# Performance work log

Measured on AMD Instinct MI355X. Metric: run time of the kernel, lower is better.

## Reference

```python
import jax, jax.numpy as jnp
import numpy as np

V = 8000; TZ = 128; TU = 256; B = 64; H = 1024; E = 512; DG = 64
GI = E + 2 * H + DG  # GRU input size = embed + z_ctx + u_ctx + degree


def _build_sparse_z(rng):
    # faithful vectorized version of get_sparse_selective_input (minus vocab SLOT branch)
    z_np = rng.integers(0, V + 10, size=(TZ, B))  # some ids >= V -> OOV copy path
    res = np.full((TZ, B, V + TZ), 1e-10, np.float32)
    w = z_np[:-1]                                   # [TZ-1, B]
    cond = (w == 2) | (w >= V)
    ti, bi = np.meshgrid(np.arange(TZ - 1), np.arange(B), indexing='ij')
    col = np.where(cond, V + ti, w)
    val = np.where(cond, np.float32(5.0), np.float32(1.0))
    res[ti + 1, bi, col] = val
    return jnp.asarray(res.transpose(1, 0, 2))      # [B, TZ, V+TZ]


def setup_inputs():
    key = jax.random.key(0)
    ks = jax.random.split(key, 16)
    s = 0.02
    iv = 1.0 / np.sqrt(H)
    return dict(
        z_enc_out=jax.random.normal(ks[0], (TZ, B, H), jnp.float32),
        u_enc_out=jax.random.normal(ks[1], (TU, B, H), jnp.float32),
        m_t_input=jax.random.randint(ks[2], (1, B), 0, V),
        degree_input=jax.random.normal(ks[3], (B, DG), jnp.float32),
        last_hidden=jax.random.normal(ks[4], (1, B, H), jnp.float32),
        sparse_z_input=_build_sparse_z(np.random.default_rng(0)),
        emb_W=jax.random.normal(ks[5], (V, E), jnp.float32) * s,
        attn_z_W=jax.random.normal(ks[6], (H, 2 * H), jnp.float32) * s,
        attn_z_b=jnp.zeros((H,), jnp.float32),
        attn_z_v=jax.random.normal(ks[7], (H,), jnp.float32) * iv,
        attn_u_W=jax.random.normal(ks[8], (H, 2 * H), jnp.float32) * s,
        attn_u_b=jnp.zeros((H,), jnp.float32),
        attn_u_v=jax.random.normal(ks[9], (H,), jnp.float32) * iv,
        gru_Wih=jax.random.normal(ks[10], (3 * H, GI), jnp.float32) * s,
        gru_Whh=jax.random.normal(ks[11], (3 * H, H), jnp.float32) * s,
        gru_bih=jnp.zeros((3 * H,), jnp.float32),
        gru_bhh=jnp.zeros((3 * H,), jnp.float32),
        proj_W=jax.random.normal(ks[12], (V, 3 * H), jnp.float32) * s,
        proj_b=jnp.zeros((V,), jnp.float32),
        copy2_W=jax.random.normal(ks[13], (H, H), jnp.float32) * s,
        copy2_b=jnp.zeros((H,), jnp.float32),
    )


def _attn(hidden, enc, W, b, v):
    # hidden [1,B,H], enc [T,B,H] -> context [1,B,H] (Bahdanau additive attention)
    enc_b = jnp.transpose(enc, (1, 0, 2))                       # [B,T,H]
    Hrep = jnp.broadcast_to(jnp.transpose(hidden, (1, 0, 2)), enc_b.shape)
    energy = jnp.tanh(jnp.concatenate([Hrep, enc_b], -1) @ W.T + b)  # [B,T,H]
    scores = jnp.einsum('bth,h->bt', energy, v)[:, None, :]    # [B,1,T]
    alpha = jax.nn.softmax(scores, axis=2)
    ctx = jnp.einsum('bit,bth->bih', alpha, enc_b)              # [B,1,H]
    return jnp.transpose(ctx, (1, 0, 2))                        # [1,B,H]


def _gru_step(x, h, Wih, Whh, bih, bhh):
    # single step, torch gate order (r, z, n)
    gi = x @ Wih.T + bih
    gh = h @ Whh.T + bhh
    ir, iz, inn = jnp.split(gi, 3, -1)
    hr, hz, hn = jnp.split(gh, 3, -1)
    r = jax.nn.sigmoid(ir + hr)
    z = jax.nn.sigmoid(iz + hz)
    n = jnp.tanh(inn + r * hn)
    return (1.0 - z) * n + z * h


def reference(z_enc_out, u_enc_out, m_t_input, degree_input, last_hidden,
              sparse_z_input, emb_W, attn_z_W, attn_z_b, attn_z_v,
              attn_u_W, attn_u_b, attn_u_v, gru_Wih, gru_Whh, gru_bih, gru_bhh,
              proj_W, proj_b, copy2_W, copy2_b):
    m_embed = emb_W[m_t_input]                                  # [1,B,E]
    z_ctx = _attn(last_hidden, z_enc_out, attn_z_W, attn_z_b, attn_z_v)  # [1,B,H]
    u_ctx = _attn(last_hidden, u_enc_out, attn_u_W, attn_u_b, attn_u_v)  # [1,B,H]
    gru_in = jnp.concatenate([m_embed, u_ctx, z_ctx, degree_input[None]], axis=2)
    gru_out = _gru_step(gru_in, last_hidden, gru_Wih, gru_Whh, gru_bih, gru_bhh)
    new_hidden = gru_out                                        # single-layer GRU, 1 step
    gen_score = (jnp.concatenate([z_ctx, u_ctx, gru_out], 2) @ proj_W.T + proj_b)[0]  # [B,V]
    # pointer copy scores over z encoder states
    z_cs = jnp.tanh(jnp.transpose(z_enc_out, (1, 0, 2)) @ copy2_W.T + copy2_b)  # [B,TZ,H]
    z_cs = jnp.einsum('bth,bh->bt', z_cs, gru_out[0])           # [B,TZ]
    m = jnp.max(z_cs, axis=1, keepdims=True)
    e = jnp.exp(z_cs - m)
    z_copy = jnp.log(jnp.einsum('bt,btv->bv', e, sparse_z_input)) + m  # [B,V+TZ]
    scores = jax.nn.softmax(jnp.concatenate([gen_score, z_copy], axis=1), axis=1)
    gen_s, zc = scores[:, :V], scores[:, V:]
    proba = jnp.concatenate([gen_s + zc[:, :V], zc[:, V:]], axis=1)  # [B, V+TZ]
    return (proba, new_hidden, gru_out)
```

## Files before the change

### kernel.cpp

```cpp
#include <hip/hip_runtime.h>
#include <cmath>

#define B64 64
#define H 1024
#define E 512
#define DG 64
#define GIN 2624
#define TZ 128
#define TU 256
#define V 8000
#define VT 8128
#define NC 16128

using bf16x8 = __attribute__((ext_vector_type(8))) short;
using f32x4  = __attribute__((ext_vector_type(4))) float;

__device__ inline unsigned pack2(float a, float b) {
    unsigned ua = __float_as_uint(a) + 0x8000u;
    unsigned ub = __float_as_uint(b) + 0x8000u;
    return __builtin_amdgcn_perm(ub, ua, 0x07060302u);
}
__device__ inline uint2 pack4(float4 v) {
    return make_uint2(pack2(v.x, v.y), pack2(v.z, v.w));
}

__device__ inline void gl_lds16(const void* gptr, void* lptr) {
    __builtin_amdgcn_global_load_lds(
        (const __attribute__((address_space(1))) void*)gptr,
        (__attribute__((address_space(3))) void*)lptr, 16, 0, 0);
}

__global__ void k_cvt(const float* __restrict__ src, int ld, int koff,
                      unsigned short* __restrict__ dst)
{
    int n = blockIdx.x, k4 = threadIdx.x * 4;
    float4 v = *(const float4*)(src + (size_t)n * ld + koff + k4);
    *(uint2*)(dst + (size_t)n * 1024 + k4) = pack4(v);
}

__global__ __launch_bounds__(256) void fused_tanh_dot_bf(
    const unsigned short* __restrict__ A,
    const unsigned short* __restrict__ W,
    const float* __restrict__ addv, int add_stride,
    const float* __restrict__ multv, int mult_stride,
    float* __restrict__ outs)
{
    __shared__ unsigned short As[128 * 32];
    __shared__ unsigned short Bs[128 * 32];
    const int tid  = threadIdx.x;
    const int wave = tid >> 6, lane = tid & 63;
    const int wm = wave >> 1, wn = wave & 1;
    const int q = lane >> 4, l16 = lane & 15;
    const int m0 = blockIdx.x * 128;
    const int n0 = blockIdx.y * 128;
    const int lrow = lane >> 2;
    const int lk   = (lane & 3) * 8;

    f32x4 acc[4][4];
#pragma unroll
    for (int i = 0; i < 4; ++i)
#pragma unroll
        for (int j = 0; j < 4; ++j) acc[i][j] = f32x4{0.f, 0.f, 0.f, 0.f};

    for (int kt = 0; kt < 32; ++kt) {
        const int k0 = kt * 32;
        __syncthreads();
#pragma unroll
        for (int j = 0; j < 2; ++j) {
            int r0 = (wave * 2 + j) * 16;
            gl_lds16(A + (size_t)(m0 + r0 + lrow) * 1024 + k0 + lk, &As[r0 * 32]);
            gl_lds16(W + (size_t)(n0 + r0 + lrow) * 1024 + k0 + lk, &Bs[r0 * 32]);
        }
        __syncthreads();
        bf16x8 af[4], bfr[4];
#pragma unroll
        for (int t = 0; t < 4; ++t) af[t]  = *(bf16x8*)&As[(wm * 64 + t * 16 + l16) * 32 + q * 8];
#pragma unroll
        for (int t = 0; t < 4; ++t) bfr[t] = *(bf16x8*)&Bs[(wn * 64 + t * 16 + l16) * 32 + q * 8];
#pragma unroll
        for (int tm = 0; tm < 4; ++tm)
#pragma unroll
            for (int tn = 0; tn < 4; ++tn)
                acc[tm][tn] = __builtin_amdgcn_mfma_f32_16x16x32_bf16(
                    af[tm], bfr[tn], acc[tm][tn], 0, 0, 0);
    }

#pragma unroll
    for (int tm = 0; tm < 4; ++tm) {
#pragma unroll
        for (int r = 0; r < 4; ++r) {
            int R = m0 + wm * 64 + tm * 16 + q * 4 + r;
            int b = R & 63;
            float s = 0.f;
#pragma unroll
            for (int tn = 0; tn < 4; ++tn) {
                int col = n0 + wn * 64 + tn * 16 + l16;
                float e = acc[tm][tn][r] + addv[(size_t)b * add_stride + col];
                s += tanhf(e) * multv[(size_t)b * mult_stride + col];
            }
            s += __shfl_xor(s, 1);
            s += __shfl_xor(s, 2);
            s += __shfl_xor(s, 4);
            s += __shfl_xor(s, 8);
            if (l16 == 0) atomicAdd(&outs[R], s);
        }
    }
}

__global__ __launch_bounds__(256) void gemm_bt_mfma(
    const float* __restrict__ A, int lda,
    const float* __restrict__ W, int ldw, int koff,
    const float* __restrict__ bias,
    float* __restrict__ C, int N,
    int ks_total, int ks_chunk)
{
    __shared__ short As[64][40];
    __shared__ short Bs[64][40];
    const int tid  = threadIdx.x;
    const int wave = tid >> 6, lane = tid & 63;
    const int wm = wave >> 1, wn = wave & 1;
    const int q = lane >> 4, l16 = lane & 15;
    const int n0 = blockIdx.x * 64;
    const int kb = blockIdx.y * ks_chunk;
    const int ke = min(kb + ks_chunk, ks_total);

    f32x4 acc[2][2];
#pragma unroll
    for (int i = 0; i < 2; ++i)
#pragma unroll
        for (int j = 0; j < 2; ++j) acc[i][j] = f32x4{0.f, 0.f, 0.f, 0.f};

    for (int ks = kb; ks < ke; ++ks) {
        const int k0 = ks * 32;
        __syncthreads();
#pragma unroll
        for (int i = 0; i < 2; ++i) {
            int slot = i * 256 + tid;
            int row  = slot >> 3;
            int kq   = (slot & 7) << 2;
            float4 a = *(const float4*)(A + (size_t)row * lda + k0 + kq);
            *(uint2*)&As[row][kq] = pack4(a);
            float4 w = *(const float4*)(W + (size_t)(n0 + row) * ldw + koff + k0 + kq);
            *(uint2*)&Bs[row][kq] = pack4(w);
        }
        __syncthreads();
        bf16x8 af[2], bfr[2];
#pragma unroll
        for (int t = 0; t < 2; ++t) af[t]  = *(bf16x8*)&As[wm * 32 + t * 16 + l16][q * 8];
#pragma unroll
        for (int t = 0; t < 2; ++t) bfr[t] = *(bf16x8*)&Bs[wn * 32 + t * 16 + l16][q * 8];
#pragma unroll
        for (int tm = 0; tm < 2; ++tm)
#pragma unroll
            for (int tn = 0; tn < 2; ++tn)
                acc[tm][tn] = __builtin_amdgcn_mfma_f32_16x16x32_bf16(
                    af[tm], bfr[tn], acc[tm][tn], 0, 0, 0);
    }

#pragma unroll
    for (int tm = 0; tm < 2; ++tm) {
#pragma unroll
        for (int r = 0; r < 4; ++r) {
            int b = wm * 32 + tm * 16 + q * 4 + r;
#pragma unroll
            for (int tn = 0; tn < 2; ++tn) {
                int n = n0 + wn * 32 + tn * 16 + l16;
                float v = acc[tm][tn][r];
                if (blockIdx.y == 0) v += bias[n];
                atomicAdd(&C[(size_t)b * N + n], v);
            }
        }
    }
}

__global__ void k_gather(const int* __restrict__ mt, const float* __restrict__ embW,
                         const float* __restrict__ degree, float* __restrict__ x)
{
    int b = blockIdx.x, tid = threadIdx.x;
    int m = mt[b];
    for (int k = tid; k < E; k += 128) x[(size_t)b * GIN + k] = embW[(size_t)m * E + k];
    if (tid < DG) x[(size_t)b * GIN + E + 2 * H + tid] = degree[b * DG + tid];
}

__global__ __launch_bounds__(256) void k_softmax_ctx(
    const float* __restrict__ scores, const float* __restrict__ enc, int T,
    float* __restrict__ x, int xoff, float* __restrict__ y, int yoff)
{
    __shared__ float red[256];
    __shared__ float al[256];
    int b = blockIdx.x, hc = blockIdx.y, tid = threadIdx.x;
    float s = (tid < T) ? scores[tid * B64 + b] : -1e30f;
    red[tid] = s; __syncthreads();
    for (int off = 128; off > 0; off >>= 1) {
        if (tid < off) red[tid] = fmaxf(red[tid], red[tid + off]);
        __syncthreads();
    }
    float mx = red[0]; __syncthreads();
    float e = (tid < T) ? expf(s - mx) : 0.f;
    red[tid] = e; __syncthreads();
    for (int off = 128; off > 0; off >>= 1) {
        if (tid < off) red[tid] += red[tid + off];
        __syncthreads();
    }
    float inv = 1.f / red[0];
    al[tid] = e * inv;
    __syncthreads();
    int h = hc * 256 + tid;
    float acc = 0.f;
    for (int t = 0; t < T; ++t) acc += al[t] * enc[((size_t)t * B64 + b) * H + h];
    x[(size_t)b * GIN + xoff + h] = acc;
    y[(size_t)b * 3072 + yoff + h] = acc;
}

__global__ void k_gate(const float* __restrict__ gi, const float* __restrict__ gh,
                       const float* __restrict__ h0, float* __restrict__ gru,
                       float* __restrict__ y, float* __restrict__ out_hid,
                       float* __restrict__ out_gru)
{
    int b = blockIdx.x, tid = threadIdx.x;
    for (int j = tid; j < H; j += 256) {
        float ir = gi[(size_t)b * 3072 + j];
        float iz = gi[(size_t)b * 3072 + H + j];
        float in_ = gi[(size_t)b * 3072 + 2 * H + j];
        float hr = gh[(size_t)b * 3072 + j];
        float hz = gh[(size_t)b * 3072 + H + j];
        float hn = gh[(size_t)b * 3072 + 2 * H + j];
        float r = 1.f / (1.f + expf(-(ir + hr)));
        float z = 1.f / (1.f + expf(-(iz + hz)));
        float n = tanhf(in_ + r * hn);
        float h = h0[(size_t)b * H + j];
        float o = (1.f - z) * n + z * h;
        gru[(size_t)b * H + j] = o;
        y[(size_t)b * 3072 + 2 * H + j] = o;
        out_hid[(size_t)b * H + j] = o;
        out_gru[(size_t)b * H + j] = o;
    }
}

__global__ void k_expw(const float* __restrict__ z_cs, float* __restrict__ ew,
                       float* __restrict__ mb)
{
    __shared__ float red[128];
    int b = blockIdx.x, t = threadIdx.x;
    float s = z_cs[t * B64 + b];
    red[t] = s; __syncthreads();
    for (int off = 64; off > 0; off >>= 1) {
        if (t < off) red[t] = fmaxf(red[t], red[t + off]);
        __syncthreads();
    }
    float m = red[0];
    ew[b * TZ + t] = expf(s - m);
    if (t == 0) mb[b] = m;
}

__global__ __launch_bounds__(256) void k_sparse(
    const float* __restrict__ sz, const float* __restrict__ ew,
    const float* __restrict__ mb, float* __restrict__ zcopy)
{
    __shared__ float es[TZ];
    int c = blockIdx.x, b = blockIdx.y, tid = threadIdx.x;
    if (tid < TZ) es[tid] = ew[b * TZ + tid];
    __syncthreads();
    if (tid >= 254) return;
    int v4 = c * 254 + tid;
    const float4* base = (const float4*)(sz + (size_t)b * TZ * VT);
    float4 acc = make_float4(0.f, 0.f, 0.f, 0.f);
    for (int t = 0; t < TZ; ++t) {
        float4 xv = base[(size_t)t * (VT / 4) + v4];
        float e = es[t];
        acc.x += e * xv.x; acc.y += e * xv.y; acc.z += e * xv.z; acc.w += e * xv.w;
    }
    float m = mb[b];
    int v = v4 * 4;
    zcopy[(size_t)b * VT + v + 0] = logf(acc.x) + m;
    zcopy[(size_t)b * VT + v + 1] = logf(acc.y) + m;
    zcopy[(size_t)b * VT + v + 2] = logf(acc.z) + m;
    zcopy[(size_t)b * VT + v + 3] = logf(acc.w) + m;
}

__global__ __launch_bounds__(1024) void k_final(
    const float* __restrict__ gen, const float* __restrict__ zcopy,
    float* __restrict__ proba)
{
    __shared__ float lg[NC];
    __shared__ float wred[16];
    int b = blockIdx.x, tid = threadIdx.x;
    int lane = tid & 63, wave = tid >> 6;
    for (int i = tid; i < V; i += 1024) lg[i] = gen[(size_t)b * V + i];
    for (int i = tid; i < VT; i += 1024) lg[V + i] = zcopy[(size_t)b * VT + i];
    __syncthreads();
    float mx = -1e30f;
    for (int i = tid; i < NC; i += 1024) mx = fmaxf(mx, lg[i]);
#pragma unroll
    for (int off = 32; off > 0; off >>= 1) mx = fmaxf(mx, __shfl_xor(mx, off));
    if (lane == 0) wred[wave] = mx;
    __syncthreads();
    mx = wred[0];
#pragma unroll
    for (int w = 1; w < 16; ++w) mx = fmaxf(mx, wred[w]);
    __syncthreads();
    float sm = 0.f;
    for (int i = tid; i < NC; i += 1024) sm += expf(lg[i] - mx);
#pragma unroll
    for (int off = 32; off > 0; off >>= 1) sm += __shfl_xor(sm, off);
    if (lane == 0) wred[wave] = sm;
    __syncthreads();
    float Z = 0.f;
#pragma unroll
    for (int w = 0; w < 16; ++w) Z += wred[w];
    float invZ = 1.f / Z;
    for (int v = tid; v < VT; v += 1024) {
        float p = expf(lg[V + v] - mx) * invZ;
        if (v < V) p += expf(lg[v] - mx) * invZ;
        proba[(size_t)b * VT + v] = p;
    }
}

extern "C" void kernel_launch(void* const* d_in, const int* in_sizes, int n_in,
                              void* d_out, int out_size, void* d_ws, size_t ws_size,
                              hipStream_t stream)
{
    const float* z_enc  = (const float*)d_in[0];
    const float* u_enc  = (const float*)d_in[1];
    const int*   mt     = (const int*)d_in[2];
    const float* degree = (const float*)d_in[3];
    const float* h0     = (const float*)d_in[4];
    const float* sz     = (const float*)d_in[5];
    const float* embW   = (const float*)d_in[6];
    const float* azW    = (const float*)d_in[7];
    const float* azb    = (const float*)d_in[8];
    const float* azv    = (const float*)d_in[9];
    const float* auW    = (const float*)d_in[10];
    const float* aub    = (const float*)d_in[11];
    const float* auv    = (const float*)d_in[12];
    const float* Wih    = (const float*)d_in[13];
    const float* Whh    = (const float*)d_in[14];
    const float* bih    = (const float*)d_in[15];
    const float* bhh    = (const float*)d_in[16];
    const float* pW     = (const float*)d_in[17];
    const float* pb     = (const float*)d_in[18];
    const float* c2W    = (const float*)d_in[19];
    const float* c2b    = (const float*)d_in[20];

    float* ws       = (float*)d_ws;
    float* scores_z = ws;
    float* scores_u = ws + 8192;
    float* z_cs     = ws + 24576;
    float* hbz      = ws + 32768;
    float* hbu      = ws + 98304;
    float* gi       = ws + 163840;
    float* gh       = ws + 360448;
    float* gen      = ws + 557056;
    float* x        = ws + 1069056;
    float* y        = ws + 1236992;
    float* gru      = ws + 1433600;
    float* ew       = ws + 1499136;
    float* mb       = ws + 1507328;
    float* zcopy    = ws + 1507392;
    unsigned short* ubf   = (unsigned short*)(ws + 2027584);
    unsigned short* zbf   = ubf + (size_t)16384 * 1024;
    unsigned short* azWbf = zbf + (size_t)8192 * 1024;
    unsigned short* auWbf = azWbf + (size_t)1024 * 1024;
    unsigned short* c2Wbf = auWbf + (size_t)1024 * 1024;

    float* out_proba = (float*)d_out;
    float* out_hid   = out_proba + (size_t)B64 * VT;
    float* out_gru   = out_hid + (size_t)B64 * H;

    hipMemsetAsync(ws, 0, 1069056 * sizeof(float), stream);

    k_cvt<<<16384, 256, 0, stream>>>(u_enc, 1024, 0, ubf);
    k_cvt<<<8192, 256, 0, stream>>>(z_enc, 1024, 0, zbf);
    k_cvt<<<1024, 256, 0, stream>>>(azW, 2048, 1024, azWbf);
    k_cvt<<<1024, 256, 0, stream>>>(auW, 2048, 1024, auWbf);
    k_cvt<<<1024, 256, 0, stream>>>(c2W, 1024, 0, c2Wbf);

    gemm_bt_mfma<<<dim3(16, 4), 256, 0, stream>>>(h0, 1024, azW, 2048, 0, azb, hbz, 1024, 32, 8);
    gemm_bt_mfma<<<dim3(16, 4), 256, 0, stream>>>(h0, 1024, auW, 2048, 0, aub, hbu, 1024, 32, 8);
    k_gather<<<64, 128, 0, stream>>>(mt, embW, degree, x);
    gemm_bt_mfma<<<dim3(48, 4), 256, 0, stream>>>(h0, 1024, Whh, 1024, 0, bhh, gh, 3072, 32, 8);

    fused_tanh_dot_bf<<<dim3(64, 8), 256, 0, stream>>>(zbf, azWbf, hbz, 1024, azv, 0, scores_z);
    fused_tanh_dot_bf<<<dim3(128, 8), 256, 0, stream>>>(ubf, auWbf, hbu, 1024, auv, 0, scores_u);

    k_softmax_ctx<<<dim3(64, 4), 256, 0, stream>>>(scores_z, z_enc, TZ, x, 1536, y, 0);
    k_softmax_ctx<<<dim3(64, 4), 256, 0, stream>>>(scores_u, u_enc, TU, x, 512, y, 1024);

    gemm_bt_mfma<<<dim3(48, 4), 256, 0, stream>>>(x, GIN, Wih, GIN, 0, bih, gi, 3072, 82, 21);
    k_gate<<<64, 256, 0, stream>>>(gi, gh, h0, gru, y, out_hid, out_gru);

    fused_tanh_dot_bf<<<dim3(64, 8), 256, 0, stream>>>(zbf, c2Wbf, c2b, 0, gru, 1024, z_cs);

    gemm_bt_mfma<<<dim3(125, 3), 256, 0, stream>>>(y, 3072, pW, 3072, 0, pb, gen, 8000, 96, 32);

    k_expw<<<64, 128, 0, stream>>>(z_cs, ew, mb);
    k_sparse<<<dim3(8, 64), 256, 0, stream>>>(sz, ew, mb, zcopy);

    k_final<<<64, 1024, 0, stream>>>(gen, zcopy, out_proba);
}
```

Baseline: 864.4 us.

## Merge conversions, fuse z-attention with copy GEMM, read bf16 encoders, use fast math

```diff
diff --git a/kernel.cpp b/kernel.cpp
--- a/kernel.cpp
+++ b/kernel.cpp
@@ -24,18 +24,36 @@
     return make_uint2(pack2(v.x, v.y), pack2(v.z, v.w));
 }
 
+__device__ inline float fast_tanh(float x) {
+    float e = __expf(2.f * x);
+    return 1.f - 2.f / (e + 1.f);
+}
+__device__ inline float fast_sig(float x) {
+    return 1.f / (1.f + __expf(-x));
+}
+
 __device__ inline void gl_lds16(const void* gptr, void* lptr) {
     __builtin_amdgcn_global_load_lds(
         (const __attribute__((address_space(1))) void*)gptr,
         (__attribute__((address_space(3))) void*)lptr, 16, 0, 0);
 }
 
-__global__ void k_cvt(const float* __restrict__ src, int ld, int koff,
-                      unsigned short* __restrict__ dst)
+__global__ void k_cvt_all(const float* __restrict__ u_enc, const float* __restrict__ z_enc,
+                          const float* __restrict__ azW, const float* __restrict__ auW,
+                          const float* __restrict__ c2W,
+                          unsigned short* __restrict__ ubf, unsigned short* __restrict__ zbf,
+                          unsigned short* __restrict__ azWbf, unsigned short* __restrict__ auWbf,
+                          unsigned short* __restrict__ c2Wbf)
 {
     int n = blockIdx.x, k4 = threadIdx.x * 4;
-    float4 v = *(const float4*)(src + (size_t)n * ld + koff + k4);
-    *(uint2*)(dst + (size_t)n * 1024 + k4) = pack4(v);
+    const float* src; unsigned short* dst; int ld, koff, r;
+    if (n < 16384)      { src = u_enc; dst = ubf;   ld = 1024; koff = 0;    r = n; }
+    else if (n < 24576) { src = z_enc; dst = zbf;   ld = 1024; koff = 0;    r = n - 16384; }
+    else if (n < 25600) { src = azW;   dst = azWbf; ld = 2048; koff = 1024; r = n - 24576; }
+    else if (n < 26624) { src = auW;   dst = auWbf; ld = 2048; koff = 1024; r = n - 25600; }
+    else                { src = c2W;   dst = c2Wbf; ld = 1024; koff = 0;    r = n - 26624; }
+    float4 v = *(const float4*)(src + (size_t)r * ld + koff + k4);
+    *(uint2*)(dst + (size_t)r * 1024 + k4) = pack4(v);
 }
 
 __global__ __launch_bounds__(256) void fused_tanh_dot_bf(
@@ -96,13 +114,101 @@
             for (int tn = 0; tn < 4; ++tn) {
                 int col = n0 + wn * 64 + tn * 16 + l16;
                 float e = acc[tm][tn][r] + addv[(size_t)b * add_stride + col];
-                s += tanhf(e) * multv[(size_t)b * mult_stride + col];
+                s += fast_tanh(e) * multv[(size_t)b * mult_stride + col];
             }
             s += __shfl_xor(s, 1);
             s += __shfl_xor(s, 2);
             s += __shfl_xor(s, 4);
             s += __shfl_xor(s, 8);
             if (l16 == 0) atomicAdd(&outs[R], s);
+        }
+    }
+}
+
+__global__ __launch_bounds__(256) void ftd_z_combo(
+    const unsigned short* __restrict__ A,
+    const unsigned short* __restrict__ Wz,
+    const float* __restrict__ hbz, const float* __restrict__ azv,
+    float* __restrict__ scores,
+    const unsigned short* __restrict__ Wc,
+    const float* __restrict__ c2b,
+    float* __restrict__ tz)
+{
+    __shared__ unsigned short As[128 * 32];
+    __shared__ unsigned short Bs[128 * 32];
+    const int tid  = threadIdx.x;
+    const int wave = tid >> 6, lane = tid & 63;
+    const int wm = wave >> 1, wn = wave & 1;
+    const int q = lane >> 4, l16 = lane & 15;
+    const int m0 = blockIdx.x * 128;
+    const bool isz = blockIdx.y < 8;
+    const int n0 = (isz ? blockIdx.y : blockIdx.y - 8) * 128;
+    const unsigned short* W = isz ? Wz : Wc;
+    const int lrow = lane >> 2;
+    const int lk   = (lane & 3) * 8;
+
+    f32x4 acc[4][4];
+#pragma unroll
+    for (int i = 0; i < 4; ++i)
+#pragma unroll
+        for (int j = 0; j < 4; ++j) acc[i][j] = f32x4{0.f, 0.f, 0.f, 0.f};
+
+    for (int kt = 0; kt < 32; ++kt) {
+        const int k0 = kt * 32;
+        __syncthreads();
+#pragma unroll
+        for (int j = 0; j < 2; ++j) {
+            int r0 = (wave * 2 + j) * 16;
+            gl_lds16(A + (size_t)(m0 + r0 + lrow) * 1024 + k0 + lk, &As[r0 * 32]);
+            gl_lds16(W + (size_t)(n0 + r0 + lrow) * 1024 + k0 + lk, &Bs[r0 * 32]);
+        }
+        __syncthreads();
+        bf16x8 af[4], bfr[4];
+#pragma unroll
+        for (int t = 0; t < 4; ++t) af[t]  = *(bf16x8*)&As[(wm * 64 + t * 16 + l16) * 32 + q * 8];
+#pragma unroll
+        for (int t = 0; t < 4; ++t) bfr[t] = *(bf16x8*)&Bs[(wn * 64 + t * 16 + l16) * 32 + q * 8];
+#pragma unroll
+        for (int tm = 0; tm < 4; ++tm)
+#pragma unroll
+            for (int tn = 0; tn < 4; ++tn)
+                acc[tm][tn] = __builtin_amdgcn_mfma_f32_16x16x32_bf16(
+                    af[tm], bfr[tn], acc[tm][tn], 0, 0, 0);
+    }
+
+    if (isz) {
+#pragma unroll
+        for (int tm = 0; tm < 4; ++tm) {
+#pragma unroll
+            for (int r = 0; r < 4; ++r) {
+                int R = m0 + wm * 64 + tm * 16 + q * 4 + r;
+                int b = R & 63;
+                float s = 0.f;
+#pragma unroll
+                for (int tn = 0; tn < 4; ++tn) {
+                    int col = n0 + wn * 64 + tn * 16 + l16;
+                    float e = acc[tm][tn][r] + hbz[(size_t)b * 1024 + col];
+                    s += fast_tanh(e) * azv[col];
+                }
+                s += __shfl_xor(s, 1);
+                s += __shfl_xor(s, 2);
+                s += __shfl_xor(s, 4);
+                s += __shfl_xor(s, 8);
+                if (l16 == 0) atomicAdd(&scores[R], s);
+            }
+        }
+    } else {
+#pragma unroll
+        for (int tm = 0; tm < 4; ++tm) {
+#pragma unroll
+            for (int r = 0; r < 4; ++r) {
+                int R = m0 + wm * 64 + tm * 16 + q * 4 + r;
+#pragma unroll
+                for (int tn = 0; tn < 4; ++tn) {
+                    int col = n0 + wn * 64 + tn * 16 + l16;
+                    tz[(size_t)R * 1024 + col] = fast_tanh(acc[tm][tn][r] + c2b[col]);
+                }
+            }
         }
     }
 }
@@ -182,8 +288,8 @@
     if (tid < DG) x[(size_t)b * GIN + E + 2 * H + tid] = degree[b * DG + tid];
 }
 
-__global__ __launch_bounds__(256) void k_softmax_ctx(
-    const float* __restrict__ scores, const float* __restrict__ enc, int T,
+__global__ __launch_bounds__(256) void k_softmax_ctx_bf(
+    const float* __restrict__ scores, const unsigned short* __restrict__ encbf, int T,
     float* __restrict__ x, int xoff, float* __restrict__ y, int yoff)
 {
     __shared__ float red[256];
@@ -196,7 +302,7 @@
         __syncthreads();
     }
     float mx = red[0]; __syncthreads();
-    float e = (tid < T) ? expf(s - mx) : 0.f;
+    float e = (tid < T) ? __expf(s - mx) : 0.f;
     red[tid] = e; __syncthreads();
     for (int off = 128; off > 0; off >>= 1) {
         if (tid < off) red[tid] += red[tid + off];
@@ -205,11 +311,18 @@
     float inv = 1.f / red[0];
     al[tid] = e * inv;
     __syncthreads();
-    int h = hc * 256 + tid;
-    float acc = 0.f;
-    for (int t = 0; t < T; ++t) acc += al[t] * enc[((size_t)t * B64 + b) * H + h];
-    x[(size_t)b * GIN + xoff + h] = acc;
-    y[(size_t)b * 3072 + yoff + h] = acc;
+    int h = hc * 512 + tid * 2;
+    float a0 = 0.f, a1 = 0.f;
+    for (int t = 0; t < T; ++t) {
+        unsigned u = *(const unsigned*)(encbf + ((size_t)t * B64 + b) * 1024 + h);
+        float w = al[t];
+        a0 += w * __uint_as_float(u << 16);
+        a1 += w * __uint_as_float(u & 0xffff0000u);
+    }
+    x[(size_t)b * GIN + xoff + h]     = a0;
+    x[(size_t)b * GIN + xoff + h + 1] = a1;
+    y[(size_t)b * 3072 + yoff + h]     = a0;
+    y[(size_t)b * 3072 + yoff + h + 1] = a1;
 }
 
 __global__ void k_gate(const float* __restrict__ gi, const float* __restrict__ gh,
@@ -225,9 +338,9 @@
         float hr = gh[(size_t)b * 3072 + j];
         float hz = gh[(size_t)b * 3072 + H + j];
         float hn = gh[(size_t)b * 3072 + 2 * H + j];
-        float r = 1.f / (1.f + expf(-(ir + hr)));
-        float z = 1.f / (1.f + expf(-(iz + hz)));
-        float n = tanhf(in_ + r * hn);
+        float r = fast_sig(ir + hr);
+        float z = fast_sig(iz + hz);
+        float n = fast_tanh(in_ + r * hn);
         float h = h0[(size_t)b * H + j];
         float o = (1.f - z) * n + z * h;
         gru[(size_t)b * H + j] = o;
@@ -237,20 +350,46 @@
     }
 }
 
-__global__ void k_expw(const float* __restrict__ z_cs, float* __restrict__ ew,
-                       float* __restrict__ mb)
-{
-    __shared__ float red[128];
-    int b = blockIdx.x, t = threadIdx.x;
-    float s = z_cs[t * B64 + b];
-    red[t] = s; __syncthreads();
-    for (int off = 64; off > 0; off >>= 1) {
-        if (t < off) red[t] = fmaxf(red[t], red[t + off]);
-        __syncthreads();
-    }
+__global__ __launch_bounds__(512) void k_zcs_expw(
+    const float* __restrict__ tz, const float* __restrict__ gru,
+    float* __restrict__ ew, float* __restrict__ mb)
+{
+    __shared__ float g[1024];
+    __shared__ float srow[TZ];
+    __shared__ float red[64];
+    int b = blockIdx.x, tid = threadIdx.x;
+    int wave = tid >> 6, lane = tid & 63;
+    for (int i = tid; i < 1024; i += 512) g[i] = gru[(size_t)b * 1024 + i];
+    __syncthreads();
+    float gr[16];
+#pragma unroll
+    for (int j = 0; j < 16; ++j) gr[j] = g[lane * 16 + j];
+    for (int t = wave; t < TZ; t += 8) {
+        const float* row = tz + ((size_t)t * B64 + b) * 1024 + lane * 16;
+        float s = 0.f;
+#pragma unroll
+        for (int c = 0; c < 4; ++c) {
+            float4 v = *(const float4*)(row + c * 4);
+            s += v.x * gr[c * 4 + 0] + v.y * gr[c * 4 + 1]
+               + v.z * gr[c * 4 + 2] + v.w * gr[c * 4 + 3];
+        }
+#pragma unroll
+        for (int off = 32; off > 0; off >>= 1) s += __shfl_xor(s, off);
+        if (lane == 0) srow[t] = s;
+    }
+    __syncthreads();
+    if (tid < 64) red[tid] = fmaxf(srow[tid], srow[tid + 64]);
+    __syncthreads();
+    if (tid < 64) {
+        float m = red[tid];
+#pragma unroll
+        for (int off = 32; off > 0; off >>= 1) m = fmaxf(m, __shfl_xor(m, off));
+        red[tid] = m;
+    }
+    __syncthreads();
     float m = red[0];
-    ew[b * TZ + t] = expf(s - m);
-    if (t == 0) mb[b] = m;
+    if (tid < TZ) ew[b * TZ + tid] = __expf(srow[tid] - m);
+    if (tid == 0) mb[b] = m;
 }
 
 __global__ __launch_bounds__(256) void k_sparse(
@@ -272,10 +411,10 @@
     }
     float m = mb[b];
     int v = v4 * 4;
-    zcopy[(size_t)b * VT + v + 0] = logf(acc.x) + m;
-    zcopy[(size_t)b * VT + v + 1] = logf(acc.y) + m;
-    zcopy[(size_t)b * VT + v + 2] = logf(acc.z) + m;
-    zcopy[(size_t)b * VT + v + 3] = logf(acc.w) + m;
+    zcopy[(size_t)b * VT + v + 0] = __logf(acc.x) + m;
+    zcopy[(size_t)b * VT + v + 1] = __logf(acc.y) + m;
+    zcopy[(size_t)b * VT + v + 2] = __logf(acc.z) + m;
+    zcopy[(size_t)b * VT + v + 3] = __logf(acc.w) + m;
 }
 
 __global__ __launch_bounds__(1024) void k_final(
@@ -300,7 +439,7 @@
     for (int w = 1; w < 16; ++w) mx = fmaxf(mx, wred[w]);
     __syncthreads();
     float sm = 0.f;
-    for (int i = tid; i < NC; i += 1024) sm += expf(lg[i] - mx);
+    for (int i = tid; i < NC; i += 1024) sm += __expf(lg[i] - mx);
 #pragma unroll
     for (int off = 32; off > 0; off >>= 1) sm += __shfl_xor(sm, off);
     if (lane == 0) wred[wave] = sm;
@@ -310,8 +449,8 @@
     for (int w = 0; w < 16; ++w) Z += wred[w];
     float invZ = 1.f / Z;
     for (int v = tid; v < VT; v += 1024) {
-        float p = expf(lg[V + v] - mx) * invZ;
-        if (v < V) p += expf(lg[v] - mx) * invZ;
+        float p = __expf(lg[V + v] - mx) * invZ;
+        if (v < V) p += __expf(lg[v] - mx) * invZ;
         proba[(size_t)b * VT + v] = p;
     }
 }
@@ -345,7 +484,6 @@
     float* ws       = (float*)d_ws;
     float* scores_z = ws;
     float* scores_u = ws + 8192;
-    float* z_cs     = ws + 24576;
     float* hbz      = ws + 32768;
     float* hbu      = ws + 98304;
     float* gi       = ws + 163840;
@@ -357,7 +495,8 @@
     float* ew       = ws + 1499136;
     float* mb       = ws + 1507328;
     float* zcopy    = ws + 1507392;
-    unsigned short* ubf   = (unsigned short*)(ws + 2027584);
+    float* tz       = ws + 2027584;
+    unsigned short* ubf   = (unsigned short*)(ws + 2027584 + 8388608);
     unsigned short* zbf   = ubf + (size_t)16384 * 1024;
     unsigned short* azWbf = zbf + (size_t)8192 * 1024;
     unsigned short* auWbf = azWbf + (size_t)1024 * 1024;
@@ -369,31 +508,28 @@
 
     hipMemsetAsync(ws, 0, 1069056 * sizeof(float), stream);
 
-    k_cvt<<<16384, 256, 0, stream>>>(u_enc, 1024, 0, ubf);
-    k_cvt<<<8192, 256, 0, stream>>>(z_enc, 1024, 0, zbf);
-    k_cvt<<<1024, 256, 0, stream>>>(azW, 2048, 1024, azWbf);
-    k_cvt<<<1024, 256, 0, stream>>>(auW, 2048, 1024, auWbf);
-    k_cvt<<<1024, 256, 0, stream>>>(c2W, 1024, 0, c2Wbf);
+    k_cvt_all<<<27648, 256, 0, stream>>>(u_enc, z_enc, azW, auW, c2W,
+                                         ubf, zbf, azWbf, auWbf, c2Wbf);
 
     gemm_bt_mfma<<<dim3(16, 4), 256, 0, stream>>>(h0, 1024, azW, 2048, 0, azb, hbz, 1024, 32, 8);
     gemm_bt_mfma<<<dim3(16, 4), 256, 0, stream>>>(h0, 1024, auW, 2048, 0, aub, hbu, 1024, 32, 8);
     k_gather<<<64, 128, 0, stream>>>(mt, embW, degree, x);
     gemm_bt_mfma<<<dim3(48, 4), 256, 0, stream>>>(h0, 1024, Whh, 1024, 0, bhh, gh, 3072, 32, 8);
 
-    fused_tanh_dot_bf<<<dim3(64, 8), 256, 0, stream>>>(zbf, azWbf, hbz, 1024, azv, 0, scores_z);
+    ftd_z_combo<<<dim3(64, 16), 256, 0, stream>>>(zbf, azWbf, hbz, azv, scores_z,
+                                                  c2Wbf, c2b, tz);
     fused_tanh_dot_bf<<<dim3(128, 8), 256, 0, stream>>>(ubf, auWbf, hbu, 1024, auv, 0, scores_u);
 
-    k_softmax_ctx<<<dim3(64, 4), 256, 0, stream>>>(scores_z, z_enc, TZ, x, 1536, y, 0);
-    k_softmax_ctx<<<dim3(64, 4), 256, 0, stream>>>(scores_u, u_enc, TU, x, 512, y, 1024);
+    k_softmax_ctx_bf<<<dim3(64, 2), 256, 0, stream>>>(scores_z, zbf, TZ, x, 1536, y, 0);
+    k_softmax_ctx_bf<<<dim3(64, 2), 256, 0, stream>>>(scores_u, ubf, TU, x, 512, y, 1024);
 
     gemm_bt_mfma<<<dim3(48, 4), 256, 0, stream>>>(x, GIN, Wih, GIN, 0, bih, gi, 3072, 82, 21);
     k_gate<<<64, 256, 0, stream>>>(gi, gh, h0, gru, y, out_hid, out_gru);
 
-    fused_tanh_dot_bf<<<dim3(64, 8), 256, 0, stream>>>(zbf, c2Wbf, c2b, 0, gru, 1024, z_cs);
+    k_zcs_expw<<<64, 512, 0, stream>>>(tz, gru, ew, mb);
 
     gemm_bt_mfma<<<dim3(125, 3), 256, 0, stream>>>(y, 3072, pW, 3072, 0, pb, gen, 8000, 96, 32);
 
-    k_expw<<<64, 128, 0, stream>>>(z_cs, ew, mb);
     k_sparse<<<dim3(8, 64), 256, 0, stream>>>(sz, ew, mb, zcopy);
 
     k_final<<<64, 1024, 0, stream>>>(gen, zcopy, out_proba);
```

New measurement: 812.4 us. 1.06x faster.
